# Performance work log

Hardware: AMD Instinct MI355X
Metric: run time of the kernel (lower is better)

Reference implementation:

```python
import jax, jax.numpy as jnp
import numpy as np

jax.config.update("jax_enable_x64", True)

B, H, W = 16384, 19, 19
MAX_FLOOD = min(H * W // 4, 100)  # = 90, as in the torch module


def _count_neighbors(m):
    # m: [B,H,W] float. Sum of 4 orthogonal neighbors (zero-padded edges).
    up = jnp.pad(m[:, :-1, :], ((0, 0), (1, 0), (0, 0)))
    down = jnp.pad(m[:, 1:, :], ((0, 0), (0, 1), (0, 0)))
    left = jnp.pad(m[:, :, :-1], ((0, 0), (0, 0), (1, 0)))
    right = jnp.pad(m[:, :, 1:], ((0, 0), (0, 0), (0, 1)))
    return up + down + left + right


def _dilate(m):
    # m: [B,H,W] bool. OR of 4 orthogonal neighbors (False-padded edges).
    up = jnp.pad(m[:, :-1, :], ((0, 0), (1, 0), (0, 0)))
    down = jnp.pad(m[:, 1:, :], ((0, 0), (0, 1), (0, 0)))
    left = jnp.pad(m[:, :, :-1], ((0, 0), (0, 0), (1, 0)))
    right = jnp.pad(m[:, :, 1:], ((0, 0), (0, 0), (0, 1)))
    return up | down | left | right


def _flood_fill(seeds, mask):
    # Iterative neighbor expansion within mask, bounded iters + early exit.
    def cond(st):
        _, changed, i = st
        return changed & (i < MAX_FLOOD)

    def body(st):
        g, _, i = st
        exp = _dilate(g) & mask & ~g
        return (g | exp, exp.any(), i + 1)

    g, _, _ = jax.lax.while_loop(cond, body, (seeds, seeds.any(), jnp.int32(0)))
    return g


def setup_inputs() -> dict:
    key = jax.random.key(0)
    k1, k2, k3, k4, k5, k6 = jax.random.split(key, 6)
    # 0 = empty, 1 = black, 2 = white (planes never overlap)
    board = jax.random.randint(k1, (B, H, W), 0, 3)
    stones = jnp.stack([board == 1, board == 2], axis=1).astype(jnp.float32)
    current_player = jax.random.randint(k2, (B,), 0, 2).astype(jnp.int32)
    ko_rc = jax.random.randint(k3, (B, 2), 0, H).astype(jnp.int32)
    has_ko = jax.random.uniform(k4, (B,)) < 0.25
    ko_points = jnp.where(has_ko[:, None], ko_rc, jnp.int32(-1))
    hmax = np.iinfo(np.int64).max
    zobrist_stones = jax.random.randint(k5, (2, H, W), 0, hmax, dtype=jnp.int64)
    zobrist_turn = jax.random.randint(k6, (2,), 0, hmax, dtype=jnp.int64)
    position_hash = jnp.zeros((B,), jnp.int64)
    return {
        "stones": stones,
        "current_player": current_player,
        "ko_points": ko_points,
        "zobrist_stones": zobrist_stones,
        "zobrist_turn": zobrist_turn,
        "position_hash": position_hash,
    }


def reference(stones, current_player, ko_points, zobrist_stones, zobrist_turn, position_hash):
    stones_b = stones > 0.5                       # [B,2,H,W] bool
    empty_f = 1.0 - stones.sum(axis=1)            # [B,H,W] float (0/1)
    empty = ~stones_b.any(axis=1)                 # empty_mask
    liberties = _count_neighbors(empty_f)         # float liberty count per point

    # legal = empty points with at least one empty neighbor
    legal = empty & (liberties > 0.0)

    # capture moves: opponent stones with exactly one liberty
    cp = current_player.astype(jnp.int32)
    opp = jnp.take_along_axis(stones_b, (1 - cp)[:, None, None, None], axis=1)[:, 0]
    vulnerable = opp & (jnp.round(liberties).astype(jnp.int32) == 1)
    cap = empty & (_count_neighbors(vulnerable.astype(jnp.float32)) > 0.0)
    legal = legal | cap

    # ko restriction: mask the single ko point per game (if set)
    valid_ko = ko_points[:, 0] >= 0
    r_eq = jnp.arange(H)[None, :, None] == ko_points[:, 0][:, None, None]
    c_eq = jnp.arange(W)[None, None, :] == ko_points[:, 1][:, None, None]
    legal = legal & ~(valid_ko[:, None, None] & r_eq & c_eq)

    # flood fill the full groups-in-atari within opponent stones
    groups = _flood_fill(vulnerable, opp)

    # zobrist hash: XOR of stone hashes over the board + turn toggle
    contrib = jnp.where(stones_b, zobrist_stones[None], jnp.int64(0))  # [B,2,H,W]
    board_hash = jax.lax.reduce(contrib, np.int64(0), jax.lax.bitwise_xor, (1, 2, 3))
    new_hash = position_hash ^ board_hash ^ zobrist_turn[cp] ^ zobrist_turn[1 - cp]

    return (liberties, legal, groups, new_hash)
```

## Files before the change

kernel.cpp:

```cpp
#include <hip/hip_runtime.h>
#include <stdint.h>

#define WW 19
#define NP 361
#define M19 0x7FFFFu
#define BPW 3
#define BPB 12
#define TPB 256
#define STGF (BPB * 722)
#define P64 40

typedef float f32x4 __attribute__((ext_vector_type(4)));

__device__ __forceinline__ uint32_t rev19(uint32_t x) { return __brev(x) >> 13; }

__device__ __forceinline__ uint32_t runfill(uint32_t g, uint32_t m) {
  const uint32_t up = g | (m & ((m + g) ^ m ^ g));
  const uint32_t rm = rev19(m);
  const uint32_t rg = rev19(g);
  const uint32_t dn = rg | (rm & ((rm + rg) ^ rm ^ rg));
  return up | rev19(dn);
}

__device__ __forceinline__ uint64_t spr3(uint32_t v) {
  uint64_t x = v;
  x = (x | (x << 32)) & 0x1f00000000ffffull;
  x = (x | (x << 16)) & 0x1f0000ff0000ffull;
  x = (x | (x << 8)) & 0x100f00f00f00f00full;
  x = (x | (x << 4)) & 0x10c30c30c30c30c3ull;
  x = (x | (x << 2)) & 0x1249249249249249ull;
  return x;
}
__device__ __forceinline__ uint64_t spr2(uint32_t v) {
  uint64_t x = v;
  x = (x | (x << 16)) & 0x0000ffff0000ffffull;
  x = (x | (x << 8)) & 0x00ff00ff00ff00ffull;
  x = (x | (x << 4)) & 0x0f0f0f0f0f0f0f0full;
  x = (x | (x << 2)) & 0x3333333333333333ull;
  x = (x | (x << 1)) & 0x5555555555555555ull;
  return x;
}

__global__ __launch_bounds__(TPB, 4) void go_fused(
    const float* __restrict__ stones, const int* __restrict__ cur,
    const int* __restrict__ ko, const int* __restrict__ zob,
    const int* __restrict__ zturn, const int* __restrict__ phash,
    float* __restrict__ out, int B) {
  __shared__ float stg[STGF];
  __shared__ uint64_t pl64[BPB * P64];

  const int wid = threadIdx.x >> 6;
  const int lane = threadIdx.x & 63;
  const int b0 = blockIdx.x * BPB;
  const int nb = min(BPB, B - b0);
  const size_t NB = (size_t)B * NP;

  int zb[6], zw[6];
#pragma unroll
  for (int i = 0; i < 6; ++i) {
    const int p = i * 64 + lane;
    zb[i] = (p < NP) ? zob[p] : 0;
    zw[i] = (p < NP) ? zob[NP + p] : 0;
  }
  const int zt = zturn[0] ^ zturn[1];

  {
    const uint32_t nfl = (uint32_t)nb * 722u;
    const float* gsrc = stones + (size_t)b0 * 722;
#pragma unroll
    for (int rnd = 0; rnd < 9; ++rnd) {
      const uint32_t fo = (uint32_t)rnd * 1024u + (uint32_t)wid * 256u +
                          (uint32_t)lane * 4u;
      if (fo < nfl) {
        __builtin_amdgcn_global_load_lds(
            (const __attribute__((address_space(1))) uint32_t*)(gsrc + fo),
            (__attribute__((address_space(3))) uint32_t*)(stg + rnd * 1024 +
                                                          wid * 256),
            16, 0, 0);
      }
    }
  }
  __syncthreads();

  {
    int hv[BPW];
#pragma unroll
    for (int k = 0; k < BPW; ++k) {
      const int lb = wid * BPW + k;
      const int base = lb * 722;
      int h = 0;
#pragma unroll
      for (int i = 0; i < 6; ++i) {
        const int cc = i * 64 + lane;
        if (cc < NP) {
          const uint32_t sb = stg[base + cc] > 0.5f;
          const uint32_t sw = stg[base + 361 + cc] > 0.5f;
          h ^= zb[i] & -(int)sb;
          h ^= zw[i] & -(int)sw;
        }
      }
      hv[k] = h;
    }
#pragma unroll
    for (int off = 32; off > 0; off >>= 1) {
#pragma unroll
      for (int k = 0; k < BPW; ++k) hv[k] ^= __shfl_xor(hv[k], off, 64);
    }
    if (lane == 0) {
#pragma unroll
      for (int k = 0; k < BPW; ++k) {
        const int b = b0 + wid * BPW + k;
        if (b < B) out[3 * NB + b] = (float)(phash[b] ^ hv[k] ^ zt);
      }
    }
  }

  {
    const int k = (lane * 27) >> 9;
    const int r = lane - k * WW;
    const int lb = wid * BPW + k;
    const int b = b0 + lb;
    const bool vl = (lane < 57) && (lb < nb);
    const int lbs = vl ? lb : 0;

    uint32_t brow = 0, wrow = 0;
    {
      const float* rb = &stg[lbs * 722 + r * WW];
#pragma unroll
      for (int c = 0; c < WW; ++c) {
        brow |= (uint32_t)(rb[c] > 0.5f) << c;
        wrow |= (uint32_t)(rb[361 + c] > 0.5f) << c;
      }
    }
    const int cp = vl ? cur[b] : 0;
    int2 kk = {-1, -1};
    if (vl) kk = ((const int2*)ko)[b];
    uint32_t mrow = (cp == 0) ? wrow : brow;
    uint32_t erow = ~(brow | wrow) & M19;
    if (!vl) { mrow = 0; erow = 0; }

    uint32_t t;
    t = __shfl(erow, lane - 1, 64);
    const uint32_t eu = (r > 0) ? t : 0u;
    t = __shfl(erow, lane + 1, 64);
    const uint32_t ed = (r < 18) ? t : 0u;
    const uint32_t el = (erow << 1) & M19;
    const uint32_t er_ = erow >> 1;
    const uint32_t s1 = eu ^ ed, c1 = eu & ed;
    const uint32_t s2 = el ^ er_, c2 = el & er_;
    const uint32_t cc = s1 & s2;
    const uint32_t L0 = s1 ^ s2;
    const uint32_t L1 = c1 ^ c2 ^ cc;
    const uint32_t L2 = (c1 & c2) | (cc & (c1 | c2));
    uint32_t leg = erow & (eu | ed | el | er_);
    const uint32_t vul = mrow & L0 & ~L1;
    t = __shfl(vul, lane - 1, 64);
    const uint32_t vu = (r > 0) ? t : 0u;
    t = __shfl(vul, lane + 1, 64);
    const uint32_t vd = (r < 18) ? t : 0u;
    leg |= erow & (vu | vd | ((vul << 1) & M19) | (vul >> 1));
    if (kk.x == r) leg &= ~(1u << kk.y);

    if (vl)
      pl64[lb * P64 + r] = spr3(L0) | (spr3(L1) << 1) | (spr3(L2) << 2);

    uint32_t g = runfill(vul, mrow);
    for (int it = 0; it < 90; ++it) {
      t = __shfl(g, lane - 1, 64);
      const uint32_t gu = (r > 0) ? t : 0u;
      t = __shfl(g, lane + 1, 64);
      const uint32_t gd = (r < 18) ? t : 0u;
      const uint32_t gn = runfill(g | ((gu | gd) & mrow), mrow);
      if (!__any(gn != g)) break;
      g = gn;
    }

    if (vl) pl64[lb * P64 + 19 + r] = spr2(leg) | (spr2(g) << 1);
  }
  __syncthreads();

  {
    const int nq = nb * NP / 4;
    f32x4* s0 = (f32x4*)(out + (size_t)b0 * NP);
    f32x4* s1 = (f32x4*)(out + NB + (size_t)b0 * NP);
    f32x4* s2 = (f32x4*)(out + 2 * NB + (size_t)b0 * NP);
    for (int q = threadIdx.x; q < nq; q += TPB) {
      f32x4 t0, t1, t2;
#pragma unroll
      for (int j = 0; j < 4; ++j) {
        const int id = q * 4 + j;
        const int lb = (int)(((uint64_t)id * 5948986ull) >> 31);
        const int p = id - lb * NP;
        const int r = (p * 27) >> 9;
        const int c = p - r * WW;
        const uint64_t lib = pl64[lb * P64 + r];
        const uint64_t lg = pl64[lb * P64 + 19 + r];
        t0[j] = (float)((uint32_t)(lib >> (3 * c)) & 7u);
        const uint32_t lgv = (uint32_t)(lg >> (2 * c));
        t1[j] = (float)(lgv & 1u);
        t2[j] = (float)((lgv >> 1) & 1u);
      }
      s0[q] = t0;
      s1[q] = t1;
      s2[q] = t2;
    }
    const int rem0 = nq * 4;
    for (int id = rem0 + threadIdx.x; id < nb * NP; id += TPB) {
      const int lb = (int)(((uint64_t)id * 5948986ull) >> 31);
      const int p = id - lb * NP;
      const int r = (p * 27) >> 9;
      const int c = p - r * WW;
      const uint64_t lib = pl64[lb * P64 + r];
      const uint64_t lg = pl64[lb * P64 + 19 + r];
      out[(size_t)b0 * NP + id] = (float)((uint32_t)(lib >> (3 * c)) & 7u);
      const uint32_t lgv = (uint32_t)(lg >> (2 * c));
      out[NB + (size_t)b0 * NP + id] = (float)(lgv & 1u);
      out[2 * NB + (size_t)b0 * NP + id] = (float)((lgv >> 1) & 1u);
    }
  }
}

extern "C" void kernel_launch(void* const* d_in, const int* in_sizes, int n_in,
                              void* d_out, int out_size, void* d_ws,
                              size_t ws_size, hipStream_t stream) {
  const float* stones = (const float*)d_in[0];
  const int* cur = (const int*)d_in[1];
  const int* ko = (const int*)d_in[2];
  const int* zob = (const int*)d_in[3];
  const int* zturn = (const int*)d_in[4];
  const int* phash = (const int*)d_in[5];
  float* out = (float*)d_out;

  const int B = in_sizes[0] / (2 * NP);
  const int blocks = (B + BPB - 1) / BPB;
  go_fused<<<blocks, TPB, 0, stream>>>(stones, cur, ko, zob, zturn, phash, out,
                                       B);
}
```

Measured before the change: 28.51 us.

## Make kernel persistent with double-buffered LDS prefetch of next board chunk

Converts the one-chunk-per-block kernel into a persistent grid of up to 512 blocks that loop over chunks of 12 boards. While the current chunk is processed, the next chunk's stones are prefetched into a second LDS buffer. The aim is to hide global load latency behind the flood-fill and output work. The cost is double the LDS per block, lower occupancy (launch bound 2), and a barrier that waits only on lgkmcnt, which may not cover the async global-to-LDS loads.

```diff
diff --git a/kernel.cpp b/kernel.cpp
--- a/kernel.cpp
+++ b/kernel.cpp
@@ -9,6 +9,7 @@
 #define TPB 256
 #define STGF (BPB * 722)
 #define P64 40
+#define GRID 512
 
 typedef float f32x4 __attribute__((ext_vector_type(4)));
 
@@ -41,19 +42,20 @@
   return x;
 }
 
-__global__ __launch_bounds__(TPB, 4) void go_fused(
+__global__ __launch_bounds__(TPB, 2) void go_pipe(
     const float* __restrict__ stones, const int* __restrict__ cur,
     const int* __restrict__ ko, const int* __restrict__ zob,
     const int* __restrict__ zturn, const int* __restrict__ phash,
     float* __restrict__ out, int B) {
-  __shared__ float stg[STGF];
+  __shared__ float stg[2][STGF];
   __shared__ uint64_t pl64[BPB * P64];
 
   const int wid = threadIdx.x >> 6;
   const int lane = threadIdx.x & 63;
-  const int b0 = blockIdx.x * BPB;
-  const int nb = min(BPB, B - b0);
   const size_t NB = (size_t)B * NP;
+  const int NCH = (B + BPB - 1) / BPB;
+
+  if (blockIdx.x >= (unsigned)NCH) return;
 
   int zb[6], zw[6];
 #pragma unroll
@@ -64,9 +66,10 @@
   }
   const int zt = zturn[0] ^ zturn[1];
 
-  {
-    const uint32_t nfl = (uint32_t)nb * 722u;
-    const float* gsrc = stones + (size_t)b0 * 722;
+  auto stage = [&](int buf, int cc) {
+    const int nbc = min(BPB, B - cc * BPB);
+    const uint32_t nfl = (uint32_t)nbc * 722u;
+    const float* gsrc = stones + (size_t)cc * BPB * 722;
 #pragma unroll
     for (int rnd = 0; rnd < 9; ++rnd) {
       const uint32_t fo = (uint32_t)rnd * 1024u + (uint32_t)wid * 256u +
@@ -74,149 +77,165 @@
       if (fo < nfl) {
         __builtin_amdgcn_global_load_lds(
             (const __attribute__((address_space(1))) uint32_t*)(gsrc + fo),
-            (__attribute__((address_space(3))) uint32_t*)(stg + rnd * 1024 +
+            (__attribute__((address_space(3))) uint32_t*)(&stg[buf][0] +
+                                                          rnd * 1024 +
                                                           wid * 256),
             16, 0, 0);
       }
     }
-  }
+  };
+
+  stage(0, blockIdx.x);
   __syncthreads();
 
-  {
-    int hv[BPW];
-#pragma unroll
-    for (int k = 0; k < BPW; ++k) {
+  int bufc = 0;
+  for (int c = blockIdx.x; c < NCH; c += GRID) {
+    const int b0 = c * BPB;
+    const int nb = min(BPB, B - b0);
+    const float* sbuf = &stg[bufc][0];
+
+    if (c + GRID < NCH) stage(bufc ^ 1, c + GRID);
+
+    {
+      int hv[BPW];
+#pragma unroll
+      for (int k = 0; k < BPW; ++k) {
+        const int lb = wid * BPW + k;
+        const int base = lb * 722;
+        int h = 0;
+#pragma unroll
+        for (int i = 0; i < 6; ++i) {
+          const int cc2 = i * 64 + lane;
+          if (cc2 < NP) {
+            const uint32_t sb = sbuf[base + cc2] > 0.5f;
+            const uint32_t sw = sbuf[base + 361 + cc2] > 0.5f;
+            h ^= zb[i] & -(int)sb;
+            h ^= zw[i] & -(int)sw;
+          }
+        }
+        hv[k] = h;
+      }
+#pragma unroll
+      for (int off = 32; off > 0; off >>= 1) {
+#pragma unroll
+        for (int k = 0; k < BPW; ++k) hv[k] ^= __shfl_xor(hv[k], off, 64);
+      }
+      if (lane == 0) {
+#pragma unroll
+        for (int k = 0; k < BPW; ++k) {
+          const int b = b0 + wid * BPW + k;
+          if (b < B) out[3 * NB + b] = (float)(phash[b] ^ hv[k] ^ zt);
+        }
+      }
+    }
+
+    {
+      const int k = (lane * 27) >> 9;
+      const int r = lane - k * WW;
       const int lb = wid * BPW + k;
-      const int base = lb * 722;
-      int h = 0;
-#pragma unroll
-      for (int i = 0; i < 6; ++i) {
-        const int cc = i * 64 + lane;
-        if (cc < NP) {
-          const uint32_t sb = stg[base + cc] > 0.5f;
-          const uint32_t sw = stg[base + 361 + cc] > 0.5f;
-          h ^= zb[i] & -(int)sb;
-          h ^= zw[i] & -(int)sw;
-        }
-      }
-      hv[k] = h;
-    }
-#pragma unroll
-    for (int off = 32; off > 0; off >>= 1) {
-#pragma unroll
-      for (int k = 0; k < BPW; ++k) hv[k] ^= __shfl_xor(hv[k], off, 64);
-    }
-    if (lane == 0) {
-#pragma unroll
-      for (int k = 0; k < BPW; ++k) {
-        const int b = b0 + wid * BPW + k;
-        if (b < B) out[3 * NB + b] = (float)(phash[b] ^ hv[k] ^ zt);
-      }
-    }
-  }
-
-  {
-    const int k = (lane * 27) >> 9;
-    const int r = lane - k * WW;
-    const int lb = wid * BPW + k;
-    const int b = b0 + lb;
-    const bool vl = (lane < 57) && (lb < nb);
-    const int lbs = vl ? lb : 0;
-
-    uint32_t brow = 0, wrow = 0;
+      const int b = b0 + lb;
+      const bool vl = (lane < 57) && (lb < nb);
+      const int lbs = vl ? lb : 0;
+
+      uint32_t brow = 0, wrow = 0;
+      {
+        const float* rb = &sbuf[lbs * 722 + r * WW];
+#pragma unroll
+        for (int cc2 = 0; cc2 < WW; ++cc2) {
+          brow |= (uint32_t)(rb[cc2] > 0.5f) << cc2;
+          wrow |= (uint32_t)(rb[361 + cc2] > 0.5f) << cc2;
+        }
+      }
+      const int cp = vl ? cur[b] : 0;
+      int2 kk = {-1, -1};
+      if (vl) kk = ((const int2*)ko)[b];
+      uint32_t mrow = (cp == 0) ? wrow : brow;
+      uint32_t erow = ~(brow | wrow) & M19;
+      if (!vl) { mrow = 0; erow = 0; }
+
+      uint32_t t;
+      t = __shfl(erow, lane - 1, 64);
+      const uint32_t eu = (r > 0) ? t : 0u;
+      t = __shfl(erow, lane + 1, 64);
+      const uint32_t ed = (r < 18) ? t : 0u;
+      const uint32_t el = (erow << 1) & M19;
+      const uint32_t er_ = erow >> 1;
+      const uint32_t s1 = eu ^ ed, c1 = eu & ed;
+      const uint32_t s2 = el ^ er_, c2 = el & er_;
+      const uint32_t cc = s1 & s2;
+      const uint32_t L0 = s1 ^ s2;
+      const uint32_t L1 = c1 ^ c2 ^ cc;
+      const uint32_t L2 = (c1 & c2) | (cc & (c1 | c2));
+      uint32_t leg = erow & (eu | ed | el | er_);
+      const uint32_t vul = mrow & L0 & ~L1;
+      t = __shfl(vul, lane - 1, 64);
+      const uint32_t vu = (r > 0) ? t : 0u;
+      t = __shfl(vul, lane + 1, 64);
+      const uint32_t vd = (r < 18) ? t : 0u;
+      leg |= erow & (vu | vd | ((vul << 1) & M19) | (vul >> 1));
+      if (kk.x == r) leg &= ~(1u << kk.y);
+
+      if (vl)
+        pl64[lb * P64 + r] = spr3(L0) | (spr3(L1) << 1) | (spr3(L2) << 2);
+
+      uint32_t g = runfill(vul, mrow);
+      for (int it = 0; it < 90; ++it) {
+        t = __shfl(g, lane - 1, 64);
+        const uint32_t gu = (r > 0) ? t : 0u;
+        t = __shfl(g, lane + 1, 64);
+        const uint32_t gd = (r < 18) ? t : 0u;
+        const uint32_t gn = runfill(g | ((gu | gd) & mrow), mrow);
+        if (!__any(gn != g)) break;
+        g = gn;
+      }
+      if (vl) pl64[lb * P64 + 19 + r] = spr2(leg) | (spr2(g) << 1);
+    }
+
+    asm volatile("s_waitcnt lgkmcnt(0)" ::: "memory");
+    __builtin_amdgcn_s_barrier();
+
     {
-      const float* rb = &stg[lbs * 722 + r * WW];
-#pragma unroll
-      for (int c = 0; c < WW; ++c) {
-        brow |= (uint32_t)(rb[c] > 0.5f) << c;
-        wrow |= (uint32_t)(rb[361 + c] > 0.5f) << c;
-      }
-    }
-    const int cp = vl ? cur[b] : 0;
-    int2 kk = {-1, -1};
-    if (vl) kk = ((const int2*)ko)[b];
-    uint32_t mrow = (cp == 0) ? wrow : brow;
-    uint32_t erow = ~(brow | wrow) & M19;
-    if (!vl) { mrow = 0; erow = 0; }
-
-    uint32_t t;
-    t = __shfl(erow, lane - 1, 64);
-    const uint32_t eu = (r > 0) ? t : 0u;
-    t = __shfl(erow, lane + 1, 64);
-    const uint32_t ed = (r < 18) ? t : 0u;
-    const uint32_t el = (erow << 1) & M19;
-    const uint32_t er_ = erow >> 1;
-    const uint32_t s1 = eu ^ ed, c1 = eu & ed;
-    const uint32_t s2 = el ^ er_, c2 = el & er_;
-    const uint32_t cc = s1 & s2;
-    const uint32_t L0 = s1 ^ s2;
-    const uint32_t L1 = c1 ^ c2 ^ cc;
-    const uint32_t L2 = (c1 & c2) | (cc & (c1 | c2));
-    uint32_t leg = erow & (eu | ed | el | er_);
-    const uint32_t vul = mrow & L0 & ~L1;
-    t = __shfl(vul, lane - 1, 64);
-    const uint32_t vu = (r > 0) ? t : 0u;
-    t = __shfl(vul, lane + 1, 64);
-    const uint32_t vd = (r < 18) ? t : 0u;
-    leg |= erow & (vu | vd | ((vul << 1) & M19) | (vul >> 1));
-    if (kk.x == r) leg &= ~(1u << kk.y);
-
-    if (vl)
-      pl64[lb * P64 + r] = spr3(L0) | (spr3(L1) << 1) | (spr3(L2) << 2);
-
-    uint32_t g = runfill(vul, mrow);
-    for (int it = 0; it < 90; ++it) {
-      t = __shfl(g, lane - 1, 64);
-      const uint32_t gu = (r > 0) ? t : 0u;
-      t = __shfl(g, lane + 1, 64);
-      const uint32_t gd = (r < 18) ? t : 0u;
-      const uint32_t gn = runfill(g | ((gu | gd) & mrow), mrow);
-      if (!__any(gn != g)) break;
-      g = gn;
-    }
-
-    if (vl) pl64[lb * P64 + 19 + r] = spr2(leg) | (spr2(g) << 1);
-  }
-  __syncthreads();
-
-  {
-    const int nq = nb * NP / 4;
-    f32x4* s0 = (f32x4*)(out + (size_t)b0 * NP);
-    f32x4* s1 = (f32x4*)(out + NB + (size_t)b0 * NP);
-    f32x4* s2 = (f32x4*)(out + 2 * NB + (size_t)b0 * NP);
-    for (int q = threadIdx.x; q < nq; q += TPB) {
-      f32x4 t0, t1, t2;
-#pragma unroll
-      for (int j = 0; j < 4; ++j) {
-        const int id = q * 4 + j;
+      const int nq = nb * NP / 4;
+      f32x4* s0 = (f32x4*)(out + (size_t)b0 * NP);
+      f32x4* s1 = (f32x4*)(out + NB + (size_t)b0 * NP);
+      f32x4* s2 = (f32x4*)(out + 2 * NB + (size_t)b0 * NP);
+      for (int q = threadIdx.x; q < nq; q += TPB) {
+        f32x4 t0, t1, t2;
+#pragma unroll
+        for (int j = 0; j < 4; ++j) {
+          const int id = q * 4 + j;
+          const int lb = (int)(((uint64_t)id * 5948986ull) >> 31);
+          const int p = id - lb * NP;
+          const int r = (p * 27) >> 9;
+          const int cc2 = p - r * WW;
+          const uint64_t lib = pl64[lb * P64 + r];
+          const uint64_t lg = pl64[lb * P64 + 19 + r];
+          t0[j] = (float)((uint32_t)(lib >> (3 * cc2)) & 7u);
+          const uint32_t lgv = (uint32_t)(lg >> (2 * cc2));
+          t1[j] = (float)(lgv & 1u);
+          t2[j] = (float)((lgv >> 1) & 1u);
+        }
+        s0[q] = t0;
+        s1[q] = t1;
+        s2[q] = t2;
+      }
+      const int rem0 = nq * 4;
+      for (int id = rem0 + threadIdx.x; id < nb * NP; id += TPB) {
         const int lb = (int)(((uint64_t)id * 5948986ull) >> 31);
         const int p = id - lb * NP;
         const int r = (p * 27) >> 9;
-        const int c = p - r * WW;
+        const int cc2 = p - r * WW;
         const uint64_t lib = pl64[lb * P64 + r];
         const uint64_t lg = pl64[lb * P64 + 19 + r];
-        t0[j] = (float)((uint32_t)(lib >> (3 * c)) & 7u);
-        const uint32_t lgv = (uint32_t)(lg >> (2 * c));
-        t1[j] = (float)(lgv & 1u);
-        t2[j] = (float)((lgv >> 1) & 1u);
-      }
-      s0[q] = t0;
-      s1[q] = t1;
-      s2[q] = t2;
-    }
-    const int rem0 = nq * 4;
-    for (int id = rem0 + threadIdx.x; id < nb * NP; id += TPB) {
-      const int lb = (int)(((uint64_t)id * 5948986ull) >> 31);
-      const int p = id - lb * NP;
-      const int r = (p * 27) >> 9;
-      const int c = p - r * WW;
-      const uint64_t lib = pl64[lb * P64 + r];
-      const uint64_t lg = pl64[lb * P64 + 19 + r];
-      out[(size_t)b0 * NP + id] = (float)((uint32_t)(lib >> (3 * c)) & 7u);
-      const uint32_t lgv = (uint32_t)(lg >> (2 * c));
-      out[NB + (size_t)b0 * NP + id] = (float)(lgv & 1u);
-      out[2 * NB + (size_t)b0 * NP + id] = (float)((lgv >> 1) & 1u);
-    }
+        out[(size_t)b0 * NP + id] = (float)((uint32_t)(lib >> (3 * cc2)) & 7u);
+        const uint32_t lgv = (uint32_t)(lg >> (2 * cc2));
+        out[NB + (size_t)b0 * NP + id] = (float)(lgv & 1u);
+        out[2 * NB + (size_t)b0 * NP + id] = (float)((lgv >> 1) & 1u);
+      }
+    }
+
+    __syncthreads();
+    bufc ^= 1;
   }
 }
 
@@ -232,7 +251,8 @@
   float* out = (float*)d_out;
 
   const int B = in_sizes[0] / (2 * NP);
-  const int blocks = (B + BPB - 1) / BPB;
-  go_fused<<<blocks, TPB, 0, stream>>>(stones, cur, ko, zob, zturn, phash, out,
-                                       B);
-}
+  const int NCH = (B + BPB - 1) / BPB;
+  const int blocks = min(GRID, NCH);
+  go_pipe<<<blocks, TPB, 0, stream>>>(stones, cur, ko, zob, zturn, phash, out,
+                                      B);
+}
```

Result: slower. 30.91 us (+8.4%).
